# Kernel tuning notes

Hardware: AMD Instinct MI355X
Metric: run time of the kernel (lower is better)

The kernel has to match this reference:

```python
import jax, jax.numpy as jnp
import numpy as np

BSZ, NW, T = 16, 1024, 3072   # batch, max words per seq, padded byte length
BED, WED = 128, 512           # byte_embed_dim, word_embed_dim
NH = 2                        # highway layers per block
VOCAB = 256 + 4 + 4
BPE_MASK_IDX = 4


def _conv1d(x, W, b):
    # x: [B, T, Cin], W: [k, Cin, Cout]
    y = jax.lax.conv_general_dilated(x, W, window_strides=(1,), padding='SAME',
                                     dimension_numbers=('NWC', 'WIO', 'NWC'))
    return y + b


def _highway(x, Ws, bs):
    # Ws: [NH, 2D, D], bs: [NH, 2D]; AllenNLP-style highway
    for i in range(NH):
        proj = x @ Ws[i].T + bs[i]
        h, g = jnp.split(proj, 2, axis=-1)
        g = jax.nn.sigmoid(g)
        x = g * jax.nn.relu(h) + (1.0 - g) * x
    return x


def setup_inputs() -> dict:
    rng = np.random.default_rng(0)
    pool_lengths = rng.integers(1, 4, size=(BSZ, NW)).astype(np.int64)  # all >=1 -> npools == NW
    src_lengths = pool_lengths.sum(axis=1)
    byte_tokens = np.zeros((BSZ, T), dtype=np.int64)
    for b in range(BSZ):
        L = int(src_lengths[b])
        byte_tokens[b, :L] = rng.integers(4, 260, size=L)
    pos = np.arange(T)[None, :]
    bpe_mask = (rng.random((BSZ, T)) < 0.3) & (pos < src_lengths[:, None])

    key = jax.random.key(0)
    ks = jax.random.split(key, 12)
    s = 0.02
    tok_emb = jax.random.normal(ks[0], (VOCAB, BED), jnp.float32) * s
    tok_emb = tok_emb.at[0].set(0.0)  # padding_idx = 0
    return {
        'byte_tokens': jnp.asarray(byte_tokens),
        'bpe_mask': jnp.asarray(bpe_mask),
        'pool_lengths': jnp.asarray(pool_lengths),
        'tok_emb': tok_emb,
        'conv0_W': jax.random.normal(ks[1], (3, BED, WED), jnp.float32) * s,
        'conv0_b': jnp.zeros((WED,), jnp.float32),
        'conv1_W': jax.random.normal(ks[2], (3, WED, WED), jnp.float32) * s,
        'conv1_b': jnp.zeros((WED,), jnp.float32),
        'hw0_W': jax.random.normal(ks[3], (NH, 2 * WED, WED), jnp.float32) * s,
        'hw0_b': jnp.zeros((NH, 2 * WED), jnp.float32),
        'hw1_W': jax.random.normal(ks[4], (NH, 2 * WED, WED), jnp.float32) * s,
        'hw1_b': jnp.zeros((NH, 2 * WED), jnp.float32),
        'proj_W': jax.random.normal(ks[5], (WED, WED), jnp.float32) * s,
        'proj_b': jnp.zeros((WED,), jnp.float32),
    }


def reference(byte_tokens, bpe_mask, pool_lengths, tok_emb,
              conv0_W, conv0_b, conv1_W, conv1_b,
              hw0_W, hw0_b, hw1_W, hw1_b, proj_W, proj_b):
    # byte embedding + bpe-marker embedding (index 0 row is zero => no-op where mask is False)
    x = tok_emb[byte_tokens] + tok_emb[jnp.where(bpe_mask, BPE_MASK_IDX, 0)]
    # ConvHighway block 0 (no residual)
    x = _highway(jax.nn.relu(_conv1d(x, conv0_W, conv0_b)), hw0_W, hw0_b)
    # ConvHighway block 1 (residual_conv=True); dropout is identity in eval
    x = _highway(jax.nn.relu(_conv1d(x, conv1_W, conv1_b)) + x, hw1_W, hw1_b)

    # ragged per-word max pool via segment_max (replaces the python double loop)
    cum = jnp.cumsum(pool_lengths, axis=1)                 # [B, NW]
    pos = jnp.arange(T)
    seg = jax.vmap(lambda c: jnp.searchsorted(c, pos, side='right'))(cum)  # [B, T]
    src_len = cum[:, -1]
    valid = pos[None, :] < src_len[:, None]
    gid = jnp.where(valid, jnp.arange(BSZ)[:, None] * NW + jnp.clip(seg, 0, NW - 1), BSZ * NW)
    pooled = jax.ops.segment_max(x.reshape(BSZ * T, WED), gid.reshape(-1),
                                 num_segments=BSZ * NW + 1)
    pooled = pooled[:BSZ * NW].reshape(BSZ, NW, WED)
    pooled = jnp.where(jnp.isfinite(pooled), pooled, 0.0)  # empty pools -> 0 like new_zeros
    return pooled @ proj_W.T + proj_b
```

## Files before the change

kernel.cpp:

```cpp
#include <hip/hip_runtime.h>
#include <hip/hip_bf16.h>
#include <math.h>

typedef __attribute__((ext_vector_type(8))) short short8v;
typedef __attribute__((ext_vector_type(4))) float float4v;

namespace {
constexpr int kBSZ = 16;
constexpr int kNW  = 1024;
constexpr int kT   = 3072;
constexpr int kBED = 128;
constexpr int kWED = 512;
constexpr int kR   = kBSZ * kT;
constexpr int kMP  = kBSZ * kNW;
}

__device__ __forceinline__ unsigned short f2b(float x) {
  unsigned int u = __float_as_uint(x);
  u = u + 0x7FFFu + ((u >> 16) & 1u);
  return (unsigned short)(u >> 16);
}
__device__ __forceinline__ float b2f(unsigned short u) {
  return __uint_as_float(((unsigned int)u) << 16);
}

__device__ __forceinline__ void async16(void* l, const void* g) {
  __builtin_amdgcn_global_load_lds(
      (const __attribute__((address_space(1))) void*)g,
      (__attribute__((address_space(3))) void*)l, 16, 0, 0);
}

__global__ __launch_bounds__(256) void k_embed(
    const int* __restrict__ tok, const int* __restrict__ msk,
    const float* __restrict__ emb, unsigned short* __restrict__ out) {
  int idx = blockIdx.x * 256 + threadIdx.x;
  int row = idx >> 5, c4 = idx & 31;
  const float4* e4 = (const float4*)emb;
  float4 a = e4[tok[row] * 32 + c4];
  float4 b = e4[(msk[row] ? 4 : 0) * 32 + c4];
  ushort4 o;
  o.x = f2b(a.x + b.x); o.y = f2b(a.y + b.y);
  o.z = f2b(a.z + b.z); o.w = f2b(a.w + b.w);
  ((ushort4*)out)[idx] = o;
}

__global__ __launch_bounds__(256) void k_wt_conv(
    const float* __restrict__ W, unsigned short* __restrict__ o, int CIN) {
  int idx = blockIdx.x * 256 + threadIdx.x;
  if (idx >= 3 * kWED * CIN) return;
  int k = idx % CIN, n = (idx / CIN) % kWED, dt = idx / (kWED * CIN);
  o[idx] = f2b(W[(long)(dt * CIN + k) * kWED + n]);
}
__global__ __launch_bounds__(256) void k_f2bk(
    const float* __restrict__ in, unsigned short* __restrict__ o, int n) {
  int idx = blockIdx.x * 256 + threadIdx.x;
  if (idx < n) o[idx] = f2b(in[idx]);
}

__global__ void k_cumsum(const int* __restrict__ pl, int* __restrict__ cum) {
  __shared__ int s[kNW];
  int b = blockIdx.x, i = threadIdx.x;
  s[i] = pl[b * kNW + i];
  __syncthreads();
  for (int off = 1; off < kNW; off <<= 1) {
    int cur = s[i];
    int add = (i >= off) ? s[i - off] : 0;
    __syncthreads();
    s[i] = cur + add;
    __syncthreads();
  }
  cum[b * kNW + i] = s[i];
}

template <int CIN, bool RESID>
__global__ __launch_bounds__(256, 2) void k_convm(
    const unsigned short* __restrict__ X,
    const unsigned short* __restrict__ Wt,
    const float* __restrict__ bias,
    const unsigned short* __restrict__ resid,
    const int* __restrict__ cum,
    unsigned short* __restrict__ out) {
  const int row0 = blockIdx.x * 128, n0 = blockIdx.y * 128;
  const int b = row0 / kT, t0 = row0 % kT;
  if (t0 >= cum[b * kNW + kNW - 1] + 2) return;

  constexpr int NT = CIN / 32;
  __shared__ short lds[2][(130 + 384) * 32];
  const int tid = threadIdx.x, wave = tid >> 6, lane = tid & 63;
  const int q = lane >> 4, rr = lane & 15;
  const int dr = lane >> 2, sl = lane & 3;
  const bool lo_ok = (t0 > 0), hi_ok = (t0 + 128 < kT);
  const int wr = (wave >> 1) * 64, wc = (wave & 1) * 64;

  float4v acc[4][4] = {};
  short8v hv = {0, 0, 0, 0, 0, 0, 0, 0};
  const int hch = tid & 3;
  const long hrow = (tid < 4) ? (long)(row0 - 1) : (long)(row0 + 128);
  const bool hok = (tid < 4) ? lo_ok : hi_ok;

  auto stage = [&](int nb, int k0) {
    short* As = lds[nb];
    short* Bs = lds[nb] + 130 * 32;
#pragma unroll
    for (int i = 0; i < 2; ++i) {
      int r0 = (wave + 4 * i) * 16;
      async16((char*)As + (1 + r0) * 64,
              X + (long)(row0 + r0 + dr) * CIN + k0 + sl * 8);
    }
#pragma unroll
    for (int i = 0; i < 6; ++i) {
      int r0 = (wave + 4 * i) * 16;
      int br = r0 + dr;
      int dt = br >> 7, n = br & 127;
      async16((char*)Bs + r0 * 64,
              Wt + ((long)(dt * kWED + n0 + n)) * CIN + k0 + sl * 8);
    }
    if (tid < 8) {
      short8v v = {0, 0, 0, 0, 0, 0, 0, 0};
      if (hok) v = *(const short8v*)(X + hrow * CIN + k0 + hch * 8);
      hv = v;
    }
  };
  auto halo_write = [&](int nb) {
    if (tid < 8) {
      int r = (tid < 4) ? 0 : 129;
      *(short8v*)((char*)lds[nb] + r * 64 + hch * 16) = hv;
    }
  };

  stage(0, 0);
  halo_write(0);
  __syncthreads();

  for (int t = 0; t < NT; ++t) {
    const int cur = t & 1, nb = cur ^ 1;
    if (t + 1 < NT) stage(nb, (t + 1) * 32);
    const char* As = (const char*)lds[cur];
    const char* Bs = (const char*)(lds[cur] + 130 * 32);
#pragma unroll
    for (int dt = 0; dt < 3; ++dt) {
      short8v a[4], bb[4];
#pragma unroll
      for (int mf = 0; mf < 4; ++mf)
        a[mf] = *(const short8v*)(As + (wr + rr + dt + mf * 16) * 64 + q * 16);
#pragma unroll
      for (int nf = 0; nf < 4; ++nf)
        bb[nf] = *(const short8v*)(Bs + (dt * 128 + wc + rr + nf * 16) * 64 + q * 16);
#pragma unroll
      for (int mf = 0; mf < 4; ++mf)
#pragma unroll
        for (int nf = 0; nf < 4; ++nf)
          acc[mf][nf] = __builtin_amdgcn_mfma_f32_16x16x32_bf16(
              a[mf], bb[nf], acc[mf][nf], 0, 0, 0);
    }
    if (t + 1 < NT) halo_write(nb);
    __syncthreads();
  }

#pragma unroll
  for (int nf = 0; nf < 4; ++nf) {
    int col = n0 + wc + nf * 16 + rr;
    float bv = bias[col];
#pragma unroll
    for (int mf = 0; mf < 4; ++mf)
#pragma unroll
      for (int r = 0; r < 4; ++r) {
        long row = row0 + wr + mf * 16 + q * 4 + r;
        float y = fmaxf(acc[mf][nf][r] + bv, 0.f);
        if (RESID) y += b2f(resid[row * kWED + col]);
        out[row * kWED + col] = f2b(y);
      }
  }
}

__global__ __launch_bounds__(256, 2) void k_hw(
    const unsigned short* __restrict__ X,
    const unsigned short* __restrict__ Wb,
    const float* __restrict__ bias,
    const int* __restrict__ cum,
    unsigned short* __restrict__ out) {
  const int row0 = blockIdx.x * 128, n0 = blockIdx.y * 128;
  const int b = row0 / kT, t0 = row0 % kT;
  if (t0 >= cum[b * kNW + kNW - 1] + 2) return;

  __shared__ short lds[2][(128 + 256) * 32];
  const int tid = threadIdx.x, wave = tid >> 6, lane = tid & 63;
  const int q = lane >> 4, rr = lane & 15;
  const int dr = lane >> 2, sl = lane & 3;
  const int wr = (wave >> 1) * 64, wc = (wave & 1) * 64;

  float4v acch[4][4] = {}, accg[4][4] = {};

  auto stage = [&](int nb, int k0) {
    short* As = lds[nb];
    short* Bs = lds[nb] + 128 * 32;
#pragma unroll
    for (int i = 0; i < 2; ++i) {
      int r0 = (wave + 4 * i) * 16;
      async16((char*)As + r0 * 64,
              X + (long)(row0 + r0 + dr) * kWED + k0 + sl * 8);
    }
#pragma unroll
    for (int i = 0; i < 4; ++i) {
      int r0 = (wave + 4 * i) * 16;
      int br = r0 + dr;
      int g = br >> 7, n = br & 127;
      async16((char*)Bs + r0 * 64,
              Wb + ((long)(g * 512 + n0 + n)) * kWED + k0 + sl * 8);
    }
  };

  stage(0, 0);
  __syncthreads();

  for (int t = 0; t < 16; ++t) {
    const int cur = t & 1, nb = cur ^ 1;
    if (t + 1 < 16) stage(nb, (t + 1) * 32);
    const char* As = (const char*)lds[cur];
    const char* Bs = (const char*)(lds[cur] + 128 * 32);
    short8v a[4], bh[4], bg[4];
#pragma unroll
    for (int mf = 0; mf < 4; ++mf)
      a[mf] = *(const short8v*)(As + (wr + rr + mf * 16) * 64 + q * 16);
#pragma unroll
    for (int nf = 0; nf < 4; ++nf) {
      bh[nf] = *(const short8v*)(Bs + (wc + rr + nf * 16) * 64 + q * 16);
      bg[nf] = *(const short8v*)(Bs + (128 + wc + rr + nf * 16) * 64 + q * 16);
    }
#pragma unroll
    for (int mf = 0; mf < 4; ++mf)
#pragma unroll
      for (int nf = 0; nf < 4; ++nf) {
        acch[mf][nf] = __builtin_amdgcn_mfma_f32_16x16x32_bf16(
            a[mf], bh[nf], acch[mf][nf], 0, 0, 0);
        accg[mf][nf] = __builtin_amdgcn_mfma_f32_16x16x32_bf16(
            a[mf], bg[nf], accg[mf][nf], 0, 0, 0);
      }
    __syncthreads();
  }

#pragma unroll
  for (int nf = 0; nf < 4; ++nf) {
    int col = n0 + wc + nf * 16 + rr;
    float bhv = bias[col], bgv = bias[512 + col];
#pragma unroll
    for (int mf = 0; mf < 4; ++mf)
#pragma unroll
      for (int r = 0; r < 4; ++r) {
        long row = row0 + wr + mf * 16 + q * 4 + r;
        float h = fmaxf(acch[mf][nf][r] + bhv, 0.f);
        float g = 1.f / (1.f + __expf(-(accg[mf][nf][r] + bgv)));
        float xv = b2f(X[row * kWED + col]);
        out[row * kWED + col] = f2b(g * h + (1.f - g) * xv);
      }
  }
}

__global__ __launch_bounds__(256, 2) void k_proj(
    const unsigned short* __restrict__ A,
    const unsigned short* __restrict__ Wb,
    const float* __restrict__ bias,
    float* __restrict__ out) {
  __shared__ short lds[2][(128 + 128) * 32];
  const int tid = threadIdx.x, wave = tid >> 6, lane = tid & 63;
  const int q = lane >> 4, rr = lane & 15;
  const int dr = lane >> 2, sl = lane & 3;
  const int row0 = blockIdx.x * 128, n0 = blockIdx.y * 128;
  const int wr = (wave >> 1) * 64, wc = (wave & 1) * 64;

  float4v acc[4][4] = {};

  auto stage = [&](int nb, int k0) {
    short* As = lds[nb];
    short* Bs = lds[nb] + 128 * 32;
#pragma unroll
    for (int i = 0; i < 2; ++i) {
      int r0 = (wave + 4 * i) * 16;
      async16((char*)As + r0 * 64,
              A + (long)(row0 + r0 + dr) * kWED + k0 + sl * 8);
    }
#pragma unroll
    for (int i = 0; i < 2; ++i) {
      int r0 = (wave + 4 * i) * 16;
      async16((char*)Bs + r0 * 64,
              Wb + (long)(n0 + r0 + dr) * kWED + k0 + sl * 8);
    }
  };

  stage(0, 0);
  __syncthreads();

  for (int t = 0; t < 16; ++t) {
    const int cur = t & 1, nb = cur ^ 1;
    if (t + 1 < 16) stage(nb, (t + 1) * 32);
    const char* As = (const char*)lds[cur];
    const char* Bs = (const char*)(lds[cur] + 128 * 32);
    short8v a[4], bb[4];
#pragma unroll
    for (int mf = 0; mf < 4; ++mf)
      a[mf] = *(const short8v*)(As + (wr + rr + mf * 16) * 64 + q * 16);
#pragma unroll
    for (int nf = 0; nf < 4; ++nf)
      bb[nf] = *(const short8v*)(Bs + (wc + rr + nf * 16) * 64 + q * 16);
#pragma unroll
    for (int mf = 0; mf < 4; ++mf)
#pragma unroll
      for (int nf = 0; nf < 4; ++nf)
        acc[mf][nf] = __builtin_amdgcn_mfma_f32_16x16x32_bf16(
            a[mf], bb[nf], acc[mf][nf], 0, 0, 0);
    __syncthreads();
  }

#pragma unroll
  for (int nf = 0; nf < 4; ++nf) {
    int col = n0 + wc + nf * 16 + rr;
    float bv = bias[col];
#pragma unroll
    for (int mf = 0; mf < 4; ++mf)
#pragma unroll
      for (int r = 0; r < 4; ++r) {
        long row = row0 + wr + mf * 16 + q * 4 + r;
        out[row * kWED + col] = acc[mf][nf][r] + bv;
      }
  }
}

__global__ __launch_bounds__(128) void k_pool(
    const unsigned short* __restrict__ x, const int* __restrict__ cum,
    unsigned short* __restrict__ pooled) {
  int bw = blockIdx.x;
  int b = bw >> 10, w = bw & 1023;
  int s = (w == 0) ? 0 : cum[bw - 1];
  int e = cum[bw];
  int c = threadIdx.x;
  float m0 = -INFINITY, m1 = -INFINITY, m2 = -INFINITY, m3 = -INFINITY;
  for (int t = s; t < e; ++t) {
    ushort4 v = ((const ushort4*)(x + (long)(b * kT + t) * kWED))[c];
    m0 = fmaxf(m0, b2f(v.x)); m1 = fmaxf(m1, b2f(v.y));
    m2 = fmaxf(m2, b2f(v.z)); m3 = fmaxf(m3, b2f(v.w));
  }
  if (e <= s) { m0 = m1 = m2 = m3 = 0.f; }
  ushort4 o;
  o.x = f2b(m0); o.y = f2b(m1); o.z = f2b(m2); o.w = f2b(m3);
  ((ushort4*)(pooled + (long)bw * kWED))[c] = o;
}

extern "C" void kernel_launch(void* const* d_in, const int* in_sizes, int n_in,
                              void* d_out, int out_size, void* d_ws, size_t ws_size,
                              hipStream_t stream) {
  (void)in_sizes; (void)n_in; (void)out_size; (void)ws_size;

  const int*   tok = (const int*)d_in[0];
  const int*   msk = (const int*)d_in[1];
  const int*   pl  = (const int*)d_in[2];
  const float* emb = (const float*)d_in[3];
  const float* c0W = (const float*)d_in[4];
  const float* c0b = (const float*)d_in[5];
  const float* c1W = (const float*)d_in[6];
  const float* c1b = (const float*)d_in[7];
  const float* h0W = (const float*)d_in[8];
  const float* h0b = (const float*)d_in[9];
  const float* h1W = (const float*)d_in[10];
  const float* h1b = (const float*)d_in[11];
  const float* pW  = (const float*)d_in[12];
  const float* pb  = (const float*)d_in[13];

  unsigned short* xb0 = (unsigned short*)d_ws;
  unsigned short* xb1 = xb0 + (size_t)kR * kWED;
  unsigned short* cw0 = xb1 + (size_t)kR * kWED;
  unsigned short* cw1 = cw0 + 3 * kWED * kBED;
  unsigned short* hw0 = cw1 + 3 * kWED * kWED;
  unsigned short* hw1 = hw0 + 2 * 1024 * kWED;
  unsigned short* pwb = hw1 + 2 * 1024 * kWED;
  int* cum = (int*)(pwb + kWED * kWED);

  k_cumsum<<<kBSZ, kNW, 0, stream>>>(pl, cum);

  k_wt_conv<<<(3 * kWED * kBED + 255) / 256, 256, 0, stream>>>(c0W, cw0, kBED);
  k_wt_conv<<<(3 * kWED * kWED + 255) / 256, 256, 0, stream>>>(c1W, cw1, kWED);
  k_f2bk<<<(2 * 1024 * kWED + 255) / 256, 256, 0, stream>>>(h0W, hw0, 2 * 1024 * kWED);
  k_f2bk<<<(2 * 1024 * kWED + 255) / 256, 256, 0, stream>>>(h1W, hw1, 2 * 1024 * kWED);
  k_f2bk<<<(kWED * kWED + 255) / 256, 256, 0, stream>>>(pW, pwb, kWED * kWED);

  k_embed<<<kR * 32 / 256, 256, 0, stream>>>(tok, msk, emb, xb0);

  dim3 g1(kR / 128, kWED / 128);

  k_convm<kBED, false><<<g1, 256, 0, stream>>>(xb0, cw0, c0b, nullptr, cum, xb1);
  k_hw<<<g1, 256, 0, stream>>>(xb1, hw0, h0b, cum, xb0);
  k_hw<<<g1, 256, 0, stream>>>(xb0, hw0 + 1024 * kWED, h0b + 1024, cum, xb1);
  k_convm<kWED, true><<<g1, 256, 0, stream>>>(xb1, cw1, c1b, xb1, cum, xb0);
  k_hw<<<g1, 256, 0, stream>>>(xb0, hw1, h1b, cum, xb1);
  k_hw<<<g1, 256, 0, stream>>>(xb1, hw1 + 1024 * kWED, h1b + 1024, cum, xb0);

  k_pool<<<kMP, 128, 0, stream>>>(xb0, cum, xb1);

  dim3 g2(kMP / 128, kWED / 128);
  k_proj<<<g2, 256, 0, stream>>>(xb1, pwb, pb, (float*)d_out);
}
```

Baseline: 429.3 us.

## Swizzle LDS tiles in GEMM kernels and merge weight-prep launches into one

Applies an XOR swizzle to the 16-byte chunk index within each 64-byte LDS row, on both the async global-to-LDS staging and the MFMA fragment reads, in the conv, highway and projection GEMMs. The aim is to reduce LDS bank conflicts on the fragment loads. It also inserts a scheduling barrier after the prefetch stage and fuses five weight-conversion kernels into a single launch to cut launch overhead. The cost is extra index arithmetic, and the swizzle only stays correct if the reader and writer mappings remain consistent, including the halo rows in the conv kernel.

```diff
diff --git a/kernel.cpp b/kernel.cpp
--- a/kernel.cpp
+++ b/kernel.cpp
@@ -29,6 +29,8 @@
       (const __attribute__((address_space(1))) void*)g,
       (__attribute__((address_space(3))) void*)l, 16, 0, 0);
 }
+
+__device__ __forceinline__ int swz(int row) { return (row >> 1) & 3; }
 
 __global__ __launch_bounds__(256) void k_embed(
     const int* __restrict__ tok, const int* __restrict__ msk,
@@ -44,17 +46,31 @@
   ((ushort4*)out)[idx] = o;
 }
 
-__global__ __launch_bounds__(256) void k_wt_conv(
-    const float* __restrict__ W, unsigned short* __restrict__ o, int CIN) {
+__global__ __launch_bounds__(256) void k_prep(
+    const float* __restrict__ c0W, const float* __restrict__ c1W,
+    const float* __restrict__ h0W, const float* __restrict__ h1W,
+    const float* __restrict__ pW,
+    unsigned short* __restrict__ cw0, unsigned short* __restrict__ cw1,
+    unsigned short* __restrict__ hw0, unsigned short* __restrict__ hw1,
+    unsigned short* __restrict__ pwb) {
   int idx = blockIdx.x * 256 + threadIdx.x;
-  if (idx >= 3 * kWED * CIN) return;
-  int k = idx % CIN, n = (idx / CIN) % kWED, dt = idx / (kWED * CIN);
-  o[idx] = f2b(W[(long)(dt * CIN + k) * kWED + n]);
-}
-__global__ __launch_bounds__(256) void k_f2bk(
-    const float* __restrict__ in, unsigned short* __restrict__ o, int n) {
-  int idx = blockIdx.x * 256 + threadIdx.x;
-  if (idx < n) o[idx] = f2b(in[idx]);
+  if (idx < 196608) {
+    int k = idx & 127, n = (idx >> 7) & 511, dt = idx >> 16;
+    cw0[idx] = f2b(c0W[(long)(dt * 128 + k) * 512 + n]);
+    return;
+  }
+  idx -= 196608;
+  if (idx < 786432) {
+    int k = idx & 511, n = (idx >> 9) & 511, dt = idx >> 18;
+    cw1[idx] = f2b(c1W[(long)(dt * 512 + k) * 512 + n]);
+    return;
+  }
+  idx -= 786432;
+  if (idx < 1048576) { hw0[idx] = f2b(h0W[idx]); return; }
+  idx -= 1048576;
+  if (idx < 1048576) { hw1[idx] = f2b(h1W[idx]); return; }
+  idx -= 1048576;
+  if (idx < 262144)  { pwb[idx] = f2b(pW[idx]); }
 }
 
 __global__ void k_cumsum(const int* __restrict__ pl, int* __restrict__ cum) {
@@ -104,16 +120,18 @@
 #pragma unroll
     for (int i = 0; i < 2; ++i) {
       int r0 = (wave + 4 * i) * 16;
+      int ch = sl ^ swz(1 + r0 + dr);
       async16((char*)As + (1 + r0) * 64,
-              X + (long)(row0 + r0 + dr) * CIN + k0 + sl * 8);
+              X + (long)(row0 + r0 + dr) * CIN + k0 + ch * 8);
     }
 #pragma unroll
     for (int i = 0; i < 6; ++i) {
       int r0 = (wave + 4 * i) * 16;
       int br = r0 + dr;
+      int ch = sl ^ swz(br);
       int dt = br >> 7, n = br & 127;
       async16((char*)Bs + r0 * 64,
-              Wt + ((long)(dt * kWED + n0 + n)) * CIN + k0 + sl * 8);
+              Wt + ((long)(dt * kWED + n0 + n)) * CIN + k0 + ch * 8);
     }
     if (tid < 8) {
       short8v v = {0, 0, 0, 0, 0, 0, 0, 0};
@@ -135,17 +153,22 @@
   for (int t = 0; t < NT; ++t) {
     const int cur = t & 1, nb = cur ^ 1;
     if (t + 1 < NT) stage(nb, (t + 1) * 32);
+    __builtin_amdgcn_sched_barrier(0);
     const char* As = (const char*)lds[cur];
     const char* Bs = (const char*)(lds[cur] + 130 * 32);
 #pragma unroll
     for (int dt = 0; dt < 3; ++dt) {
       short8v a[4], bb[4];
 #pragma unroll
-      for (int mf = 0; mf < 4; ++mf)
-        a[mf] = *(const short8v*)(As + (wr + rr + dt + mf * 16) * 64 + q * 16);
-#pragma unroll
-      for (int nf = 0; nf < 4; ++nf)
-        bb[nf] = *(const short8v*)(Bs + (dt * 128 + wc + rr + nf * 16) * 64 + q * 16);
+      for (int mf = 0; mf < 4; ++mf) {
+        int ra = wr + rr + dt + mf * 16;
+        a[mf] = *(const short8v*)(As + ra * 64 + ((q ^ swz(ra)) * 16));
+      }
+#pragma unroll
+      for (int nf = 0; nf < 4; ++nf) {
+        int rb = dt * 128 + wc + rr + nf * 16;
+        bb[nf] = *(const short8v*)(Bs + rb * 64 + ((q ^ swz(rb)) * 16));
+      }
 #pragma unroll
       for (int mf = 0; mf < 4; ++mf)
 #pragma unroll
@@ -197,16 +220,18 @@
 #pragma unroll
     for (int i = 0; i < 2; ++i) {
       int r0 = (wave + 4 * i) * 16;
+      int ch = sl ^ swz(r0 + dr);
       async16((char*)As + r0 * 64,
-              X + (long)(row0 + r0 + dr) * kWED + k0 + sl * 8);
+              X + (long)(row0 + r0 + dr) * kWED + k0 + ch * 8);
     }
 #pragma unroll
     for (int i = 0; i < 4; ++i) {
       int r0 = (wave + 4 * i) * 16;
       int br = r0 + dr;
+      int ch = sl ^ swz(br);
       int g = br >> 7, n = br & 127;
       async16((char*)Bs + r0 * 64,
-              Wb + ((long)(g * 512 + n0 + n)) * kWED + k0 + sl * 8);
+              Wb + ((long)(g * 512 + n0 + n)) * kWED + k0 + ch * 8);
     }
   };
 
@@ -216,16 +241,21 @@
   for (int t = 0; t < 16; ++t) {
     const int cur = t & 1, nb = cur ^ 1;
     if (t + 1 < 16) stage(nb, (t + 1) * 32);
+    __builtin_amdgcn_sched_barrier(0);
     const char* As = (const char*)lds[cur];
     const char* Bs = (const char*)(lds[cur] + 128 * 32);
     short8v a[4], bh[4], bg[4];
 #pragma unroll
-    for (int mf = 0; mf < 4; ++mf)
-      a[mf] = *(const short8v*)(As + (wr + rr + mf * 16) * 64 + q * 16);
+    for (int mf = 0; mf < 4; ++mf) {
+      int ra = wr + rr + mf * 16;
+      a[mf] = *(const short8v*)(As + ra * 64 + ((q ^ swz(ra)) * 16));
+    }
 #pragma unroll
     for (int nf = 0; nf < 4; ++nf) {
-      bh[nf] = *(const short8v*)(Bs + (wc + rr + nf * 16) * 64 + q * 16);
-      bg[nf] = *(const short8v*)(Bs + (128 + wc + rr + nf * 16) * 64 + q * 16);
+      int rh = wc + rr + nf * 16;
+      int rg = 128 + rh;
+      bh[nf] = *(const short8v*)(Bs + rh * 64 + ((q ^ swz(rh)) * 16));
+      bg[nf] = *(const short8v*)(Bs + rg * 64 + ((q ^ swz(rg)) * 16));
     }
 #pragma unroll
     for (int mf = 0; mf < 4; ++mf)
@@ -276,14 +306,16 @@
 #pragma unroll
     for (int i = 0; i < 2; ++i) {
       int r0 = (wave + 4 * i) * 16;
+      int ch = sl ^ swz(r0 + dr);
       async16((char*)As + r0 * 64,
-              A + (long)(row0 + r0 + dr) * kWED + k0 + sl * 8);
+              A + (long)(row0 + r0 + dr) * kWED + k0 + ch * 8);
     }
 #pragma unroll
     for (int i = 0; i < 2; ++i) {
       int r0 = (wave + 4 * i) * 16;
+      int ch = sl ^ swz(r0 + dr);
       async16((char*)Bs + r0 * 64,
-              Wb + (long)(n0 + r0 + dr) * kWED + k0 + sl * 8);
+              Wb + (long)(n0 + r0 + dr) * kWED + k0 + ch * 8);
     }
   };
 
@@ -293,15 +325,20 @@
   for (int t = 0; t < 16; ++t) {
     const int cur = t & 1, nb = cur ^ 1;
     if (t + 1 < 16) stage(nb, (t + 1) * 32);
+    __builtin_amdgcn_sched_barrier(0);
     const char* As = (const char*)lds[cur];
     const char* Bs = (const char*)(lds[cur] + 128 * 32);
     short8v a[4], bb[4];
 #pragma unroll
-    for (int mf = 0; mf < 4; ++mf)
-      a[mf] = *(const short8v*)(As + (wr + rr + mf * 16) * 64 + q * 16);
-#pragma unroll
-    for (int nf = 0; nf < 4; ++nf)
-      bb[nf] = *(const short8v*)(Bs + (wc + rr + nf * 16) * 64 + q * 16);
+    for (int mf = 0; mf < 4; ++mf) {
+      int ra = wr + rr + mf * 16;
+      a[mf] = *(const short8v*)(As + ra * 64 + ((q ^ swz(ra)) * 16));
+    }
+#pragma unroll
+    for (int nf = 0; nf < 4; ++nf) {
+      int rb = wc + rr + nf * 16;
+      bb[nf] = *(const short8v*)(Bs + rb * 64 + ((q ^ swz(rb)) * 16));
+    }
 #pragma unroll
     for (int mf = 0; mf < 4; ++mf)
 #pragma unroll
@@ -376,11 +413,8 @@
 
   k_cumsum<<<kBSZ, kNW, 0, stream>>>(pl, cum);
 
-  k_wt_conv<<<(3 * kWED * kBED + 255) / 256, 256, 0, stream>>>(c0W, cw0, kBED);
-  k_wt_conv<<<(3 * kWED * kWED + 255) / 256, 256, 0, stream>>>(c1W, cw1, kWED);
-  k_f2bk<<<(2 * 1024 * kWED + 255) / 256, 256, 0, stream>>>(h0W, hw0, 2 * 1024 * kWED);
-  k_f2bk<<<(2 * 1024 * kWED + 255) / 256, 256, 0, stream>>>(h1W, hw1, 2 * 1024 * kWED);
-  k_f2bk<<<(kWED * kWED + 255) / 256, 256, 0, stream>>>(pW, pwb, kWED * kWED);
+  k_prep<<<(3342336 + 255) / 256, 256, 0, stream>>>(
+      c0W, c1W, h0W, h1W, pW, cw0, cw1, hw0, hw1, pwb);
 
   k_embed<<<kR * 32 / 256, 256, 0, stream>>>(tok, msk, emb, xb0);
 
```

Result: faster. 399.8 us (-6.9%).
